# Kernel tuning notes

Measured on AMD Instinct MI355X. Metric: run time of the kernel, lower is better.

Reference implementation:

```python
import jax, jax.numpy as jnp
import numpy as np

DMODEL = 1024
N_EXPERTS = 16
EXPERT_SIZE = 256
K = 4


def setup_inputs() -> dict:
    key = jax.random.key(0)
    k1, k2, k3, k4 = jax.random.split(key, 4)
    std_sel = 1.0 / np.sqrt(DMODEL)
    std_val = 1.0 / np.sqrt(N_EXPERTS * EXPERT_SIZE)
    return {
        "x": jax.random.normal(k1, (4, 2048, DMODEL), dtype=jnp.float32),
        "expert_sel": jax.random.normal(k2, (N_EXPERTS, DMODEL), dtype=jnp.float32) * std_sel,
        "keys": jax.random.normal(k3, (N_EXPERTS, DMODEL, EXPERT_SIZE), dtype=jnp.float32) * std_sel,
        "values": jax.random.normal(k4, (N_EXPERTS, EXPERT_SIZE, DMODEL), dtype=jnp.float32) * std_val,
        "route_scale": jnp.ones((1,), dtype=jnp.float32),
    }


def reference(x, expert_sel, keys, values, route_scale):
    # Routing: sigmoid gating, top-k selection (eval mode: no dropout/bias balancing)
    sel_logits = jnp.einsum("btd,ed->bte", x, expert_sel)  # [B,T,E]
    sel_probs = jax.nn.sigmoid(sel_logits)
    _, sel_index = jax.lax.top_k(sel_probs, K)  # [B,T,K]
    sel_val = jnp.take_along_axis(sel_probs, sel_index, axis=-1)  # [B,T,K]
    sel_val = sel_val / jnp.clip(sel_val.sum(-1, keepdims=True), 1e-9)
    sel_val = sel_val * route_scale  # route_scale shape [1] broadcasts
    # Dense all-expert FFN (as in original), then gather top-k and combine
    scores_all = jax.nn.relu(jnp.einsum("btd,edh->bteh", x, keys))  # [B,T,E,H]
    values_all = jnp.einsum("bteh,ehv->btev", scores_all, values)   # [B,T,E,V]
    sel_idx_exp = sel_index[..., None]  # [B,T,K,1]
    selected = jnp.take_along_axis(values_all, sel_idx_exp, axis=2)  # [B,T,K,V]
    out = (selected * sel_val[..., None]).sum(axis=2)  # [B,T,V]
    return out
```

## Files before the change

kernel.cpp:

```cpp
#include <hip/hip_runtime.h>
#include <math.h>


constexpr int NTOK = 8192;
constexpr int DM   = 1024;
constexpr int NE   = 16;
constexpr int EH   = 256;
constexpr int TK   = 4;
constexpr int CAP  = 8192;
constexpr int BM   = 128;

typedef __attribute__((ext_vector_type(8))) short short8;
typedef __attribute__((ext_vector_type(4))) float f32x4;

#define MFMA16(a, b, c) __builtin_amdgcn_mfma_f32_16x16x32_bf16(a, b, c, 0, 0, 0)

__device__ __forceinline__ void gload_lds16(const void* g, void* l) {
    __builtin_amdgcn_global_load_lds(
        (const __attribute__((address_space(1))) void*)g,
        (__attribute__((address_space(3))) void*)l, 16, 0, 0);
}

__device__ __forceinline__ unsigned short f2bf(float f) {
    union { float f; unsigned int u; } x; x.f = f;
    unsigned int r = x.u + 0x7fffu + ((x.u >> 16) & 1u);
    return (unsigned short)(r >> 16);
}
__device__ __forceinline__ float bf2f(unsigned short b) {
    union { unsigned int u; float f; } x; x.u = ((unsigned int)b) << 16;
    return x.f;
}

__global__ __launch_bounds__(256) void route_conv_kernel(
    const float* __restrict__ x, const float* __restrict__ esel,
    const float* __restrict__ rscale,
    unsigned short* __restrict__ xb,
    int4* __restrict__ sel4, float* __restrict__ wtk)
{
    __shared__ float Es[NE * DM];
    int tid = threadIdx.x;

    {
        const float4* src = (const float4*)esel;
        float4* dst = (float4*)Es;
        #pragma unroll
        for (int j = 0; j < 16; ++j) dst[tid + j * 256] = src[tid + j * 256];
    }
    __syncthreads();

    int t    = blockIdx.x * 8 + (tid >> 5);
    int l32  = tid & 31;

    float acc[NE];
    #pragma unroll
    for (int e = 0; e < NE; ++e) acc[e] = 0.f;

    const float4* x4 = (const float4*)(x + (size_t)t * DM);
    const float4* E4 = (const float4*)Es;
    #pragma unroll
    for (int i4 = 0; i4 < 8; ++i4) {
        int d4 = i4 * 32 + l32;
        float4 xv = x4[d4];
        ushort4 cb = { f2bf(xv.x), f2bf(xv.y), f2bf(xv.z), f2bf(xv.w) };
        *(ushort4*)(xb + (size_t)t * DM + d4 * 4) = cb;
        #pragma unroll
        for (int e = 0; e < NE; ++e) {
            float4 wv = E4[e * 256 + d4];
            acc[e] = fmaf(xv.x, wv.x, acc[e]);
            acc[e] = fmaf(xv.y, wv.y, acc[e]);
            acc[e] = fmaf(xv.z, wv.z, acc[e]);
            acc[e] = fmaf(xv.w, wv.w, acc[e]);
        }
    }

    #pragma unroll
    for (int off = 16; off; off >>= 1)
        #pragma unroll
        for (int e = 0; e < NE; ++e)
            acc[e] += __shfl_xor(acc[e], off, 32);

    if (l32 == 0) {
        float p[NE];
        #pragma unroll
        for (int e = 0; e < NE; ++e) p[e] = 1.0f / (1.0f + expf(-acc[e]));

        int   sel_e[TK];
        float sel_p[TK];
        float sum = 0.f;
        #pragma unroll
        for (int k = 0; k < TK; ++k) {
            float best = -INFINITY; int be = NE;
            #pragma unroll
            for (int e = 0; e < NE; ++e) {
                bool take = p[e] > best;
                best = take ? p[e] : best;
                be   = take ? e    : be;
            }
            sel_e[k] = be; sel_p[k] = best; sum += best;
            #pragma unroll
            for (int e = 0; e < NE; ++e) p[e] = (e == be) ? -INFINITY : p[e];
        }

        float wsc = rscale[0] / fmaxf(sum, 1e-9f);
        int4 s = { sel_e[0], sel_e[1], sel_e[2], sel_e[3] };
        sel4[t] = s;
        float4 wv = { sel_p[0] * wsc, sel_p[1] * wsc,
                      sel_p[2] * wsc, sel_p[3] * wsc };
        *(float4*)(wtk + t * TK) = wv;
    }
}

__global__ __launch_bounds__(1024) void compact_kernel(
    const int4* __restrict__ sel4, int* __restrict__ counts,
    int* __restrict__ lpk)
{
    __shared__ int wsum[16];
    int e    = blockIdx.x;
    int tid  = threadIdx.x;
    int w    = tid >> 6;
    int lane = tid & 63;

    int base = 0;
    for (int c = 0; c < NTOK; c += 1024) {
        int t = c + tid;
        int4 s = sel4[t];
        int k = -1;
        if      (s.x == e) k = 0;
        else if (s.y == e) k = 1;
        else if (s.z == e) k = 2;
        else if (s.w == e) k = 3;
        unsigned long long m = __ballot(k >= 0);
        int rank = __popcll(m & ((1ull << lane) - 1ull));
        if (lane == 63) wsum[w] = __popcll(m);
        __syncthreads();
        int prefix = 0, total = 0;
        #pragma unroll
        for (int i = 0; i < 16; ++i) {
            int v = wsum[i];
            prefix += (i < w) ? v : 0;
            total  += v;
        }
        if (k >= 0) lpk[e * CAP + base + prefix + rank] = t * TK + k;
        base += total;
        __syncthreads();
    }
    if (tid == 0) counts[e] = base;
}

__global__ __launch_bounds__(256) void trans_kernel(
    const float* __restrict__ in, unsigned short* __restrict__ outp, int R, int C)
{
    __shared__ float T[32][33];
    int e = blockIdx.z;
    int r0 = blockIdx.y * 32, c0 = blockIdx.x * 32;
    int ri = threadIdx.x >> 3, cq = threadIdx.x & 7;
    float4 v = *(const float4*)(in + ((size_t)e * R + r0 + ri) * C + c0 + cq * 4);
    T[ri][cq * 4 + 0] = v.x; T[ri][cq * 4 + 1] = v.y;
    T[ri][cq * 4 + 2] = v.z; T[ri][cq * 4 + 3] = v.w;
    __syncthreads();
    int ci = threadIdx.x >> 3, rq = threadIdx.x & 7;
    ushort4 o = { f2bf(T[rq * 4 + 0][ci]), f2bf(T[rq * 4 + 1][ci]),
                  f2bf(T[rq * 4 + 2][ci]), f2bf(T[rq * 4 + 3][ci]) };
    *(ushort4*)(outp + ((size_t)e * C + c0 + ci) * R + r0 + rq * 4) = o;
}

template<int USE_SCRATCH>
__global__ __launch_bounds__(512, 2) void ffn_kernel(
    const unsigned short* __restrict__ xb,
    const unsigned short* __restrict__ ktb,
    const unsigned short* __restrict__ vtb,
    const int* __restrict__ counts, const int* __restrict__ lpk,
    const float* __restrict__ wtk,
    unsigned short* __restrict__ scratch,
    float* __restrict__ out)
{
    int bid = blockIdx.x;
    int xcd = bid & 7, idx = bid >> 3;
    int e   = xcd * 2 + (idx >> 6);
    int t0  = (idx & 63) * BM;
    int cnt = counts[e];
    if (t0 >= cnt) return;

    __shared__ __align__(16) char L[116224];
    char* const Xs0 = L;
    char* const Xs1 = L + 8192;
    char* const Ks0 = L + 16384;
    char* const Ks1 = L + 32768;
    char* const Ss  = L + 49152;
    int*   stok = (int*)(L + 114688);
    int*   spk  = (int*)(L + 115200);
    float* sw   = (float*)(L + 115712);

    int tid  = threadIdx.x;
    int lane = tid & 63;
    int w    = tid >> 6;
    int lm   = lane & 15;
    int q    = lane >> 4;
    int th   = w >> 2;
    int hq   = w & 3;

    if (tid < BM) {
        int s = t0 + tid;
        if (s < cnt) {
            int pk = lpk[e * CAP + s];
            stok[tid] = pk >> 2; spk[tid] = pk; sw[tid] = wtk[pk];
        } else {
            stok[tid] = 0; spk[tid] = USE_SCRATCH ? (NTOK * TK) : 0; sw[tid] = 0.f;
        }
    }
    __syncthreads();

    int rowX = tid >> 2;
    int cb   = ((tid & 3) * 16) ^ (((rowX >> 1) & 3) << 4);
    const unsigned short* kbase = ktb + (size_t)e * EH * DM;
    const unsigned short* vbase = vtb + (size_t)e * DM * EH;
    const unsigned short* srcX  = xb + (size_t)stok[rowX] * DM + (cb >> 1);
    const unsigned short* srcK0 = kbase + (size_t)rowX * DM + (cb >> 1);
    const unsigned short* srcK1 = kbase + (size_t)(rowX + 128) * DM + (cb >> 1);
    const unsigned short* srcV0 = vbase + (size_t)rowX * EH + (cb >> 1);
    const unsigned short* srcV1 = vbase + (size_t)(rowX + 128) * EH + (cb >> 1);

    auto stage1 = [&](char* Xd, char* Kd, int kc) {
        gload_lds16(srcX + kc,  Xd + w * 1024);
        gload_lds16(srcK0 + kc, Kd + w * 1024);
        gload_lds16(srcK1 + kc, Kd + 8192 + w * 1024);
    };
    auto stageV = [&](char* Kd, int nb, int kc) {
        gload_lds16(srcV0 + nb * 256 * EH + kc, Kd + w * 1024);
        gload_lds16(srcV1 + nb * 256 * EH + kc, Kd + 8192 + w * 1024);
    };

    f32x4 zero = {0.f, 0.f, 0.f, 0.f};
    f32x4 acc[4][4];
    #pragma unroll
    for (int mi = 0; mi < 4; ++mi)
        #pragma unroll
        for (int ni = 0; ni < 4; ++ni) acc[mi][ni] = zero;

    auto comp1 = [&](const char* Xb, const char* Kb) {
        short8 a[4], bb[4];
        #pragma unroll
        for (int mi = 0; mi < 4; ++mi) {
            int row = th * 64 + mi * 16 + lm;
            a[mi] = *(const short8*)(Xb + row * 64 +
                     ((q * 16) ^ (((row >> 1) & 3) << 4)));
        }
        #pragma unroll
        for (int ni = 0; ni < 4; ++ni) {
            int row = hq * 64 + ni * 16 + lm;
            bb[ni] = *(const short8*)(Kb + row * 64 +
                      ((q * 16) ^ (((row >> 1) & 3) << 4)));
        }
        #pragma unroll
        for (int mi = 0; mi < 4; ++mi)
            #pragma unroll
            for (int ni = 0; ni < 4; ++ni)
                acc[mi][ni] = MFMA16(a[mi], bb[ni], acc[mi][ni]);
    };

    stage1(Xs0, Ks0, 0);
    __syncthreads();
    for (int s2 = 0; s2 < 16; ++s2) {
        int kc = s2 * 64;
        stage1(Xs1, Ks1, kc + 32);
        comp1(Xs0, Ks0);
        __syncthreads();
        if (s2 < 15) stage1(Xs0, Ks0, kc + 64);
        else         stageV(Ks0, 0, 0);
        comp1(Xs1, Ks1);
        __syncthreads();
    }

    #pragma unroll
    for (int mi = 0; mi < 4; ++mi)
        #pragma unroll
        for (int ni = 0; ni < 4; ++ni) {
            f32x4 v = acc[mi][ni];
            #pragma unroll
            for (int r = 0; r < 4; ++r) {
                int row = th * 64 + mi * 16 + q * 4 + r;
                int col = hq * 64 + ni * 16 + lm;
                *(unsigned short*)(Ss + row * 512 +
                    ((col * 2) ^ ((row & 7) << 4))) = f2bf(fmaxf(v[r], 0.f));
            }
        }
    __syncthreads();

    int spk_[4][4];
    float sw_[4][4];
    int stok_[4][4];
    #pragma unroll
    for (int mi = 0; mi < 4; ++mi)
        #pragma unroll
        for (int r = 0; r < 4; ++r) {
            int slot = th * 64 + mi * 16 + q * 4 + r;
            spk_[mi][r] = spk[slot];
            if (!USE_SCRATCH) { sw_[mi][r] = sw[slot]; stok_[mi][r] = stok[slot]; }
        }

    int dq = hq;
    for (int nb = 0; nb < 4; ++nb) {
        f32x4 acc2[4][4];
        #pragma unroll
        for (int mi = 0; mi < 4; ++mi)
            #pragma unroll
            for (int ni = 0; ni < 4; ++ni) acc2[mi][ni] = zero;

        auto comp2 = [&](int kc, const char* Vb) {
            short8 a[4], bb[4];
            #pragma unroll
            for (int mi = 0; mi < 4; ++mi) {
                int row = th * 64 + mi * 16 + lm;
                a[mi] = *(const short8*)(Ss + row * 512 +
                         ((kc * 64 + q * 16) ^ ((row & 7) << 4)));
            }
            #pragma unroll
            for (int ni = 0; ni < 4; ++ni) {
                int row = dq * 64 + ni * 16 + lm;
                bb[ni] = *(const short8*)(Vb + row * 64 +
                          ((q * 16) ^ (((row >> 1) & 3) << 4)));
            }
            #pragma unroll
            for (int mi = 0; mi < 4; ++mi)
                #pragma unroll
                for (int ni = 0; ni < 4; ++ni)
                    acc2[mi][ni] = MFMA16(a[mi], bb[ni], acc2[mi][ni]);
        };

        #pragma unroll
        for (int kc8 = 0; kc8 < 8; kc8 += 2) {
            stageV(Ks1, nb, (kc8 + 1) * 32);
            comp2(kc8, Ks0);
            __syncthreads();
            if (kc8 < 6)      stageV(Ks0, nb, (kc8 + 2) * 32);
            else if (nb < 3)  stageV(Ks0, nb + 1, 0);
            comp2(kc8 + 1, Ks1);
            __syncthreads();
        }

        #pragma unroll
        for (int mi = 0; mi < 4; ++mi)
            #pragma unroll
            for (int ni = 0; ni < 4; ++ni) {
                f32x4 v = acc2[mi][ni];
                #pragma unroll
                for (int r = 0; r < 4; ++r) {
                    int d = nb * 256 + dq * 64 + ni * 16 + lm;
                    if (USE_SCRATCH) {
                        scratch[(size_t)spk_[mi][r] * DM + d] = f2bf(v[r]);
                    } else {
                        atomicAdd(out + (size_t)stok_[mi][r] * DM + d,
                                  sw_[mi][r] * v[r]);
                    }
                }
            }
    }
}

__global__ __launch_bounds__(256) void combine_kernel(
    const unsigned short* __restrict__ scratch, const float* __restrict__ wtk,
    float* __restrict__ out)
{
    int t  = blockIdx.x * 2 + (threadIdx.x >> 7);
    int d0 = (threadIdx.x & 127) * 8;
    float o[8] = {0.f, 0.f, 0.f, 0.f, 0.f, 0.f, 0.f, 0.f};
    #pragma unroll
    for (int k = 0; k < TK; ++k) {
        float wv = wtk[t * TK + k];
        uint4 qv = *(const uint4*)(scratch + (size_t)(t * TK + k) * DM + d0);
        unsigned int us[4] = {qv.x, qv.y, qv.z, qv.w};
        #pragma unroll
        for (int j = 0; j < 4; ++j) {
            o[j * 2 + 0] = fmaf(wv, bf2f((unsigned short)(us[j] & 0xffff)), o[j * 2 + 0]);
            o[j * 2 + 1] = fmaf(wv, bf2f((unsigned short)(us[j] >> 16)),    o[j * 2 + 1]);
        }
    }
    float4 w0 = {o[0], o[1], o[2], o[3]}, w1 = {o[4], o[5], o[6], o[7]};
    *(float4*)(out + (size_t)t * DM + d0)     = w0;
    *(float4*)(out + (size_t)t * DM + d0 + 4) = w1;
}

extern "C" void kernel_launch(void* const* d_in, const int* in_sizes, int n_in,
                              void* d_out, int out_size, void* d_ws, size_t ws_size,
                              hipStream_t stream) {
    const float* x      = (const float*)d_in[0];
    const float* esel   = (const float*)d_in[1];
    const float* keys   = (const float*)d_in[2];
    const float* values = (const float*)d_in[3];
    const float* rscale = (const float*)d_in[4];
    float* out = (float*)d_out;

    char* ws = (char*)d_ws;
    size_t o = 0;
    auto alloc = [&](size_t sz) { size_t r = o; o = (o + sz + 255) & ~(size_t)255; return r; };
    size_t o_counts = alloc(NE * 4);
    size_t o_lpk    = alloc((size_t)NE * CAP * 4);
    size_t o_sel4   = alloc((size_t)NTOK * 16);
    size_t o_wtk    = alloc((size_t)NTOK * TK * 4);
    size_t o_xb     = alloc((size_t)NTOK * DM * 2);
    size_t o_ktb    = alloc((size_t)NE * EH * DM * 2);
    size_t o_vtb    = alloc((size_t)NE * DM * EH * 2);
    size_t o_scr    = alloc(((size_t)NTOK * TK + BM) * DM * 2);
    size_t need_full = o;

    int*            counts  = (int*)(ws + o_counts);
    int*            lpk     = (int*)(ws + o_lpk);
    int4*           sel4    = (int4*)(ws + o_sel4);
    float*          wtk     = (float*)(ws + o_wtk);
    unsigned short* xb      = (unsigned short*)(ws + o_xb);
    unsigned short* ktb     = (unsigned short*)(ws + o_ktb);
    unsigned short* vtb     = (unsigned short*)(ws + o_vtb);
    unsigned short* scratch = (unsigned short*)(ws + o_scr);

    bool use_scratch = ws_size >= need_full;

    if (!use_scratch)
        hipMemsetAsync(d_out, 0, (size_t)out_size * sizeof(float), stream);

    route_conv_kernel<<<NTOK / 8, 256, 0, stream>>>(x, esel, rscale, xb,
                                                    sel4, wtk);
    compact_kernel<<<NE, 1024, 0, stream>>>(sel4, counts, lpk);
    trans_kernel<<<dim3(EH / 32, DM / 32, NE), 256, 0, stream>>>(keys, ktb, DM, EH);
    trans_kernel<<<dim3(DM / 32, EH / 32, NE), 256, 0, stream>>>(values, vtb, EH, DM);

    if (use_scratch) {
        ffn_kernel<1><<<1024, 512, 0, stream>>>(
            xb, ktb, vtb, counts, lpk, wtk, scratch, out);
        combine_kernel<<<NTOK / 2, 256, 0, stream>>>(scratch, wtk, out);
    } else {
        ffn_kernel<0><<<1024, 512, 0, stream>>>(
            xb, ktb, vtb, counts, lpk, wtk, scratch, out);
    }
}
```

Measured before the change: 144.0 us.

## Use persistent FFN blocks with triple-buffered LDS pipeline and fine-grained waits

The FFN kernel becomes persistent: 384 blocks each loop over the 128-token tiles of their expert pair, instead of launching 1024 blocks where many exit early. Global-to-LDS staging moves from double to triple buffering, with explicit vmcnt waits and raw s_barrier in place of __syncthreads, so loads run two stages ahead. MFMA sections are wrapped in s_setprio. The aim is to cut wasted block launches and barrier stalls and to overlap memory with compute better. The cost is more LDS per block, which may limit occupancy, and hand-written wait counts that are easy to get wrong.

```diff
diff --git a/kernel.cpp b/kernel.cpp
--- a/kernel.cpp
+++ b/kernel.cpp
@@ -14,6 +14,10 @@
 typedef __attribute__((ext_vector_type(4))) float f32x4;
 
 #define MFMA16(a, b, c) __builtin_amdgcn_mfma_f32_16x16x32_bf16(a, b, c, 0, 0, 0)
+#define VMCNT(n) asm volatile("s_waitcnt vmcnt(" #n ")" ::: "memory")
+#define LGKM0    asm volatile("s_waitcnt lgkmcnt(0)" ::: "memory")
+#define SBAR     __builtin_amdgcn_s_barrier()
+#define SCHED0   __builtin_amdgcn_sched_barrier(0)
 
 __device__ __forceinline__ void gload_lds16(const void* g, void* l) {
     __builtin_amdgcn_global_load_lds(
@@ -174,22 +178,13 @@
     unsigned short* __restrict__ scratch,
     float* __restrict__ out)
 {
-    int bid = blockIdx.x;
-    int xcd = bid & 7, idx = bid >> 3;
-    int e   = xcd * 2 + (idx >> 6);
-    int t0  = (idx & 63) * BM;
-    int cnt = counts[e];
-    if (t0 >= cnt) return;
-
-    __shared__ __align__(16) char L[116224];
-    char* const Xs0 = L;
-    char* const Xs1 = L + 8192;
-    char* const Ks0 = L + 16384;
-    char* const Ks1 = L + 32768;
-    char* const Ss  = L + 49152;
-    int*   stok = (int*)(L + 114688);
-    int*   spk  = (int*)(L + 115200);
-    float* sw   = (float*)(L + 115712);
+    constexpr int BUF  = 24576;
+    constexpr int META = 3 * BUF + 65536;
+    __shared__ __align__(16) char L[3 * BUF + 65536 + 1536];
+    char* const Ss = L + 3 * BUF;
+    int*   stok = (int*)(L + META);
+    int*   spk  = (int*)(L + META + 512);
+    float* sw   = (float*)(L + META + 1024);
 
     int tid  = threadIdx.x;
     int lane = tid & 63;
@@ -199,161 +194,183 @@
     int th   = w >> 2;
     int hq   = w & 3;
 
-    if (tid < BM) {
-        int s = t0 + tid;
-        if (s < cnt) {
-            int pk = lpk[e * CAP + s];
-            stok[tid] = pk >> 2; spk[tid] = pk; sw[tid] = wtk[pk];
-        } else {
-            stok[tid] = 0; spk[tid] = USE_SCRATCH ? (NTOK * TK) : 0; sw[tid] = 0.f;
-        }
-    }
-    __syncthreads();
-
-    int rowX = tid >> 2;
-    int cb   = ((tid & 3) * 16) ^ (((rowX >> 1) & 3) << 4);
-    const unsigned short* kbase = ktb + (size_t)e * EH * DM;
-    const unsigned short* vbase = vtb + (size_t)e * DM * EH;
-    const unsigned short* srcX  = xb + (size_t)stok[rowX] * DM + (cb >> 1);
-    const unsigned short* srcK0 = kbase + (size_t)rowX * DM + (cb >> 1);
-    const unsigned short* srcK1 = kbase + (size_t)(rowX + 128) * DM + (cb >> 1);
-    const unsigned short* srcV0 = vbase + (size_t)rowX * EH + (cb >> 1);
-    const unsigned short* srcV1 = vbase + (size_t)(rowX + 128) * EH + (cb >> 1);
-
-    auto stage1 = [&](char* Xd, char* Kd, int kc) {
-        gload_lds16(srcX + kc,  Xd + w * 1024);
-        gload_lds16(srcK0 + kc, Kd + w * 1024);
-        gload_lds16(srcK1 + kc, Kd + 8192 + w * 1024);
-    };
-    auto stageV = [&](char* Kd, int nb, int kc) {
-        gload_lds16(srcV0 + nb * 256 * EH + kc, Kd + w * 1024);
-        gload_lds16(srcV1 + nb * 256 * EH + kc, Kd + 8192 + w * 1024);
-    };
-
-    f32x4 zero = {0.f, 0.f, 0.f, 0.f};
-    f32x4 acc[4][4];
-    #pragma unroll
-    for (int mi = 0; mi < 4; ++mi)
-        #pragma unroll
-        for (int ni = 0; ni < 4; ++ni) acc[mi][ni] = zero;
-
-    auto comp1 = [&](const char* Xb, const char* Kb) {
-        short8 a[4], bb[4];
-        #pragma unroll
-        for (int mi = 0; mi < 4; ++mi) {
-            int row = th * 64 + mi * 16 + lm;
-            a[mi] = *(const short8*)(Xb + row * 64 +
-                     ((q * 16) ^ (((row >> 1) & 3) << 4)));
-        }
-        #pragma unroll
-        for (int ni = 0; ni < 4; ++ni) {
-            int row = hq * 64 + ni * 16 + lm;
-            bb[ni] = *(const short8*)(Kb + row * 64 +
-                      ((q * 16) ^ (((row >> 1) & 3) << 4)));
-        }
+    int xp = blockIdx.x & 7;
+    int j0 = blockIdx.x >> 3;
+    int e0 = xp * 2;
+    int c0 = counts[e0], c1 = counts[e0 + 1];
+    int n0 = (c0 + BM - 1) >> 7;
+    int ntot = n0 + ((c1 + BM - 1) >> 7);
+
+    for (int jt = j0; jt < ntot; jt += 48) {
+        int e, t0, cnt;
+        if (jt < n0) { e = e0;     t0 = jt << 7;        cnt = c0; }
+        else         { e = e0 + 1; t0 = (jt - n0) << 7; cnt = c1; }
+
+        if (tid < BM) {
+            int s = t0 + tid;
+            if (s < cnt) {
+                int pk = lpk[e * CAP + s];
+                stok[tid] = pk >> 2; spk[tid] = pk; sw[tid] = wtk[pk];
+            } else {
+                stok[tid] = 0; spk[tid] = USE_SCRATCH ? (NTOK * TK) : 0; sw[tid] = 0.f;
+            }
+        }
+        LGKM0;
+        SBAR;
+        SCHED0;
+
+        int rowX = tid >> 2;
+        int cb   = ((tid & 3) * 16) ^ (((rowX >> 1) & 3) << 4);
+        const unsigned short* kbase = ktb + (size_t)e * EH * DM;
+        const unsigned short* vbase = vtb + (size_t)e * DM * EH;
+        const unsigned short* srcX  = xb + (size_t)stok[rowX] * DM + (cb >> 1);
+        const unsigned short* srcK0 = kbase + (size_t)rowX * DM + (cb >> 1);
+        const unsigned short* srcK1 = kbase + (size_t)(rowX + 128) * DM + (cb >> 1);
+        const unsigned short* srcV0 = vbase + (size_t)rowX * EH + (cb >> 1);
+        const unsigned short* srcV1 = vbase + (size_t)(rowX + 128) * EH + (cb >> 1);
+
+        auto stage1 = [&](char* buf, int kc) {
+            gload_lds16(srcX + kc,  buf + w * 1024);
+            gload_lds16(srcK0 + kc, buf + 8192 + w * 1024);
+            gload_lds16(srcK1 + kc, buf + 16384 + w * 1024);
+        };
+        auto stageV = [&](char* buf, int nb, int kc) {
+            gload_lds16(srcV0 + nb * 256 * EH + kc, buf + w * 1024);
+            gload_lds16(srcV1 + nb * 256 * EH + kc, buf + 8192 + w * 1024);
+        };
+
+        f32x4 zero = {0.f, 0.f, 0.f, 0.f};
+        f32x4 acc[4][4];
         #pragma unroll
         for (int mi = 0; mi < 4; ++mi)
             #pragma unroll
-            for (int ni = 0; ni < 4; ++ni)
-                acc[mi][ni] = MFMA16(a[mi], bb[ni], acc[mi][ni]);
-    };
-
-    stage1(Xs0, Ks0, 0);
-    __syncthreads();
-    for (int s2 = 0; s2 < 16; ++s2) {
-        int kc = s2 * 64;
-        stage1(Xs1, Ks1, kc + 32);
-        comp1(Xs0, Ks0);
-        __syncthreads();
-        if (s2 < 15) stage1(Xs0, Ks0, kc + 64);
-        else         stageV(Ks0, 0, 0);
-        comp1(Xs1, Ks1);
-        __syncthreads();
-    }
-
-    #pragma unroll
-    for (int mi = 0; mi < 4; ++mi)
-        #pragma unroll
-        for (int ni = 0; ni < 4; ++ni) {
-            f32x4 v = acc[mi][ni];
-            #pragma unroll
-            for (int r = 0; r < 4; ++r) {
-                int row = th * 64 + mi * 16 + q * 4 + r;
-                int col = hq * 64 + ni * 16 + lm;
-                *(unsigned short*)(Ss + row * 512 +
-                    ((col * 2) ^ ((row & 7) << 4))) = f2bf(fmaxf(v[r], 0.f));
-            }
-        }
-    __syncthreads();
-
-    int spk_[4][4];
-    float sw_[4][4];
-    int stok_[4][4];
-    #pragma unroll
-    for (int mi = 0; mi < 4; ++mi)
-        #pragma unroll
-        for (int r = 0; r < 4; ++r) {
-            int slot = th * 64 + mi * 16 + q * 4 + r;
-            spk_[mi][r] = spk[slot];
-            if (!USE_SCRATCH) { sw_[mi][r] = sw[slot]; stok_[mi][r] = stok[slot]; }
-        }
-
-    int dq = hq;
-    for (int nb = 0; nb < 4; ++nb) {
-        f32x4 acc2[4][4];
-        #pragma unroll
-        for (int mi = 0; mi < 4; ++mi)
-            #pragma unroll
-            for (int ni = 0; ni < 4; ++ni) acc2[mi][ni] = zero;
-
-        auto comp2 = [&](int kc, const char* Vb) {
+            for (int ni = 0; ni < 4; ++ni) acc[mi][ni] = zero;
+
+        auto comp1 = [&](const char* buf) {
+            const char* Kb = buf + 8192;
             short8 a[4], bb[4];
             #pragma unroll
             for (int mi = 0; mi < 4; ++mi) {
                 int row = th * 64 + mi * 16 + lm;
-                a[mi] = *(const short8*)(Ss + row * 512 +
-                         ((kc * 64 + q * 16) ^ ((row & 7) << 4)));
+                a[mi] = *(const short8*)(buf + row * 64 +
+                         ((q * 16) ^ (((row >> 1) & 3) << 4)));
             }
             #pragma unroll
             for (int ni = 0; ni < 4; ++ni) {
-                int row = dq * 64 + ni * 16 + lm;
-                bb[ni] = *(const short8*)(Vb + row * 64 +
+                int row = hq * 64 + ni * 16 + lm;
+                bb[ni] = *(const short8*)(Kb + row * 64 +
                           ((q * 16) ^ (((row >> 1) & 3) << 4)));
             }
             #pragma unroll
             for (int mi = 0; mi < 4; ++mi)
                 #pragma unroll
                 for (int ni = 0; ni < 4; ++ni)
-                    acc2[mi][ni] = MFMA16(a[mi], bb[ni], acc2[mi][ni]);
+                    acc[mi][ni] = MFMA16(a[mi], bb[ni], acc[mi][ni]);
         };
 
-        #pragma unroll
-        for (int kc8 = 0; kc8 < 8; kc8 += 2) {
-            stageV(Ks1, nb, (kc8 + 1) * 32);
-            comp2(kc8, Ks0);
-            __syncthreads();
-            if (kc8 < 6)      stageV(Ks0, nb, (kc8 + 2) * 32);
-            else if (nb < 3)  stageV(Ks0, nb + 1, 0);
-            comp2(kc8 + 1, Ks1);
-            __syncthreads();
-        }
+        stage1(L, 0);
+        stage1(L + BUF, 32);
+        for (int n = 0; n < 30; ++n) {
+            VMCNT(3); SBAR; SCHED0;
+            stage1(L + ((n + 2) % 3) * BUF, (n + 2) * 32);
+            __builtin_amdgcn_s_setprio(1);
+            comp1(L + (n % 3) * BUF);
+            __builtin_amdgcn_s_setprio(0);
+        }
+        VMCNT(3); SBAR; SCHED0;
+        stageV(L + 2 * BUF, 0, 0);
+        __builtin_amdgcn_s_setprio(1);
+        comp1(L);
+        __builtin_amdgcn_s_setprio(0);
+        VMCNT(2); SBAR; SCHED0;
+        stageV(L, 0, 32);
+        __builtin_amdgcn_s_setprio(1);
+        comp1(L + BUF);
+        __builtin_amdgcn_s_setprio(0);
 
         #pragma unroll
         for (int mi = 0; mi < 4; ++mi)
             #pragma unroll
             for (int ni = 0; ni < 4; ++ni) {
-                f32x4 v = acc2[mi][ni];
+                f32x4 v = acc[mi][ni];
                 #pragma unroll
                 for (int r = 0; r < 4; ++r) {
-                    int d = nb * 256 + dq * 64 + ni * 16 + lm;
-                    if (USE_SCRATCH) {
-                        scratch[(size_t)spk_[mi][r] * DM + d] = f2bf(v[r]);
-                    } else {
-                        atomicAdd(out + (size_t)stok_[mi][r] * DM + d,
-                                  sw_[mi][r] * v[r]);
+                    int row = th * 64 + mi * 16 + q * 4 + r;
+                    int col = hq * 64 + ni * 16 + lm;
+                    *(unsigned short*)(Ss + row * 512 +
+                        ((col * 2) ^ ((row & 7) << 4))) = f2bf(fmaxf(v[r], 0.f));
+                }
+            }
+        LGKM0;
+
+        int   spk_[4][4];
+        float sw_[4][4];
+        int   stok_[4][4];
+        #pragma unroll
+        for (int mi = 0; mi < 4; ++mi)
+            #pragma unroll
+            for (int r = 0; r < 4; ++r) {
+                int slot = th * 64 + mi * 16 + q * 4 + r;
+                spk_[mi][r] = spk[slot];
+                if (!USE_SCRATCH) { sw_[mi][r] = sw[slot]; stok_[mi][r] = stok[slot]; }
+            }
+
+        for (int nb = 0; nb < 4; ++nb) {
+            f32x4 acc2[4][4];
+            #pragma unroll
+            for (int mi = 0; mi < 4; ++mi)
+                #pragma unroll
+                for (int ni = 0; ni < 4; ++ni) acc2[mi][ni] = zero;
+
+            #pragma unroll
+            for (int j2 = 0; j2 < 8; ++j2) {
+                int u = nb * 8 + j2;
+                if (u == 31) { VMCNT(0); } else { VMCNT(2); }
+                SBAR; SCHED0;
+                if (u < 30) {
+                    int u2 = u + 2;
+                    stageV(L + ((u + 1) % 3) * BUF, u2 >> 3, (u2 & 7) * 32);
+                }
+                const char* Vb = L + ((u + 2) % 3) * BUF;
+                short8 a[4], bb[4];
+                #pragma unroll
+                for (int mi = 0; mi < 4; ++mi) {
+                    int row = th * 64 + mi * 16 + lm;
+                    a[mi] = *(const short8*)(Ss + row * 512 +
+                             ((j2 * 64 + q * 16) ^ ((row & 7) << 4)));
+                }
+                #pragma unroll
+                for (int ni = 0; ni < 4; ++ni) {
+                    int row = hq * 64 + ni * 16 + lm;
+                    bb[ni] = *(const short8*)(Vb + row * 64 +
+                              ((q * 16) ^ (((row >> 1) & 3) << 4)));
+                }
+                __builtin_amdgcn_s_setprio(1);
+                #pragma unroll
+                for (int mi = 0; mi < 4; ++mi)
+                    #pragma unroll
+                    for (int ni = 0; ni < 4; ++ni)
+                        acc2[mi][ni] = MFMA16(a[mi], bb[ni], acc2[mi][ni]);
+                __builtin_amdgcn_s_setprio(0);
+            }
+
+            #pragma unroll
+            for (int mi = 0; mi < 4; ++mi)
+                #pragma unroll
+                for (int ni = 0; ni < 4; ++ni) {
+                    f32x4 v = acc2[mi][ni];
+                    #pragma unroll
+                    for (int r = 0; r < 4; ++r) {
+                        int d = nb * 256 + hq * 64 + ni * 16 + lm;
+                        if (USE_SCRATCH) {
+                            scratch[(size_t)spk_[mi][r] * DM + d] = f2bf(v[r]);
+                        } else {
+                            atomicAdd(out + (size_t)stok_[mi][r] * DM + d,
+                                      sw_[mi][r] * v[r]);
+                        }
                     }
                 }
-            }
+        }
     }
 }
 
@@ -424,11 +441,11 @@
     trans_kernel<<<dim3(DM / 32, EH / 32, NE), 256, 0, stream>>>(values, vtb, EH, DM);
 
     if (use_scratch) {
-        ffn_kernel<1><<<1024, 512, 0, stream>>>(
+        ffn_kernel<1><<<384, 512, 0, stream>>>(
             xb, ktb, vtb, counts, lpk, wtk, scratch, out);
         combine_kernel<<<NTOK / 2, 256, 0, stream>>>(scratch, wtk, out);
     } else {
-        ffn_kernel<0><<<1024, 512, 0, stream>>>(
+        ffn_kernel<0><<<384, 512, 0, stream>>>(
             xb, ktb, vtb, counts, lpk, wtk, scratch, out);
     }
 }
```

Result: faster. 140.0 us (-2.8%).
